# Optimization experiments

Measured on AMD Instinct MI355X. Metric: run time of the kernel, lower is better.

The kernel has to match this reference:

```python
import jax, jax.numpy as jnp
import numpy as np
from jax import lax

B, N, T = 64, 50, 30          # batch, history length, words per title
VOCAB, E = 50000, 300          # vocab size, word emb dim
FN, A, G, K = 400, 200, 400, 3 # filter_num, attention_dim, gru_unit, window size
USERS = 50000


def setup_inputs() -> dict:
    key = jax.random.key(0)
    ks = jax.random.split(key, 12)
    return {
        "user_id": jax.random.randint(ks[0], (B,), 0, USERS),
        "history_title": jax.random.randint(ks[1], (B, N, T), 0, VOCAB),
        "history_length": jax.random.randint(ks[2], (B,), 1, N + 1),
        "word_emb": jax.random.normal(ks[3], (VOCAB, E), jnp.float32) * 0.02,
        "conv_w": jax.random.normal(ks[4], (K, E, FN), jnp.float32) * 0.05,  # WIO layout
        "conv_b": jnp.zeros((FN,), jnp.float32),
        "v": jax.random.normal(ks[5], (FN, A), jnp.float32) * 0.05,
        "vb": jnp.zeros((A,), jnp.float32),
        "q": jax.random.normal(ks[6], (A, 1), jnp.float32) * 0.05,
        "user_emb": jax.random.normal(ks[7], (USERS, G), jnp.float32) * 0.02,
        "W_ih": jax.random.normal(ks[8], (3 * G, FN), jnp.float32) * 0.05,
        "W_hh": jax.random.normal(ks[9], (3 * G, G), jnp.float32) * 0.05,
        "b_ih": jnp.zeros((3 * G,), jnp.float32),
        "b_hh": jnp.zeros((3 * G,), jnp.float32),
    }


def _news_encode(history_title, word_emb, conv_w, conv_b, v, vb, q):
    # word embedding lookup: [B, N, T, E] (dropout is identity in eval mode)
    W = word_emb[history_title]
    # Conv1d over the word axis, padding=1 keeps length T
    x = W.reshape(B * N, T, E)
    C = lax.conv_general_dilated(
        x, conv_w, window_strides=(1,), padding=[(1, 1)],
        dimension_numbers=("NWC", "WIO", "NWC")) + conv_b
    C = jax.nn.relu(C).reshape(B, N, T, FN)
    # additive attention scores
    a = jnp.tanh(jnp.einsum("bntf,fa->bnta", C, v) + vb)
    a = jnp.einsum("bnta,ao->bnt", a, q)  # q: [A,1] -> squeeze
    # original uses Softmax(dim=0) on a [n, t] per sample => over the n-titles axis
    alpha = jax.nn.softmax(a, axis=1)
    # e[i] = alpha[i] @ C[i]: weighted sum over words -> [B, N, FN]
    return jnp.einsum("bnt,bntf->bnf", alpha, C)


def _gru(news_embed, h0, lengths, W_ih, W_hh, b_ih, b_hh):
    # packed_padded semantics: h stops updating once step >= length
    xs = jnp.swapaxes(news_embed, 0, 1)                 # [N, B, FN]
    mask = jnp.arange(N)[:, None] < lengths[None, :]    # [N, B]

    def step(h, inp):
        x_t, m = inp
        gx = x_t @ W_ih.T + b_ih                        # [B, 3G]
        gh = h @ W_hh.T + b_hh
        xr, xz, xn = jnp.split(gx, 3, axis=-1)
        hr, hz, hn = jnp.split(gh, 3, axis=-1)
        r = jax.nn.sigmoid(xr + hr)
        z = jax.nn.sigmoid(xz + hz)
        n = jnp.tanh(xn + r * hn)
        h_new = (1.0 - z) * n + z * h
        h = jnp.where(m[:, None], h_new, h)
        return h, None

    h_final, _ = lax.scan(step, h0, (xs, mask))
    return h_final


def reference(user_id, history_title, history_length, word_emb, conv_w, conv_b,
              v, vb, q, user_emb, W_ih, W_hh, b_ih, b_hh):
    news_embed = _news_encode(history_title, word_emb, conv_w, conv_b, v, vb, q)
    h0 = user_emb[user_id]                              # [B, G]
    return _gru(news_embed, h0, history_length, W_ih, W_hh, b_ih, b_hh)
```

## Files before the change

kernel.cpp:

```cpp
#include <hip/hip_runtime.h>
#include <hip/hip_bf16.h>

#define BB 64
#define NN 50
#define TT 30
#define EE 300
#define FN 400
#define AA 200
#define GG 400

typedef __attribute__((ext_vector_type(8))) short bf16x8;
typedef __attribute__((ext_vector_type(4))) float f32x4;

__global__ void k_pack_whh(const float* __restrict__ Whh, float* __restrict__ Wpack) {
  int idx = blockIdx.x * 256 + threadIdx.x;
  if (idx < 8 * 400 * 150) {
    int jl = idx % 150;
    int g = (idx / 150) % 400;
    int gc = idx / (150 * 400);
    int gate = jl / 50, gl = jl - gate * 50;
    int j = gate * 400 + gc * 50 + gl;
    Wpack[idx] = Whh[j * 400 + g];
  }
}

__global__ void k_prep_emb(const float* __restrict__ w, __hip_bfloat16* __restrict__ o) {
  long i = (long)blockIdx.x * 256 + threadIdx.x;
  if (i < (long)50000 * 320) {
    int row = (int)(i / 320), c = (int)(i % 320);
    o[i] = __float2bfloat16(c < EE ? w[(long)row * EE + c] : 0.f);
  }
}

__global__ void k_prep_wt(const float* __restrict__ cw, __hip_bfloat16* __restrict__ o) {
  int i = blockIdx.x * 256 + threadIdx.x;
  if (i < 448 * 960) {
    int f = i / 960, kk = i % 960;
    int ko = kk / 320, e = kk % 320;
    float val = (f < FN && e < EE) ? cw[(ko * EE + e) * FN + f] : 0.f;
    o[i] = __float2bfloat16(val);
  }
}

__global__ void k_prep_v(const float* __restrict__ v, __hip_bfloat16* __restrict__ o) {
  int i = blockIdx.x * 256 + threadIdx.x;
  if (i < 224 * 416) {
    int a = i / 416, f = i % 416;
    o[i] = __float2bfloat16((a < AA && f < FN) ? v[f * AA + a] : 0.f);
  }
}

__global__ void k_prep_qvb(const float* __restrict__ q, const float* __restrict__ vb,
                           float* __restrict__ qp, float* __restrict__ vbp) {
  int i = threadIdx.x;
  if (i < 224) {
    qp[i]  = i < AA ? q[i]  : 0.f;
    vbp[i] = i < AA ? vb[i] : 0.f;
  }
}

__global__ void k_prep_wih(const float* __restrict__ w, __hip_bfloat16* __restrict__ o) {
  int i = blockIdx.x * 256 + threadIdx.x;
  if (i < 1344 * 416) {
    int j = i / 416, f = i % 416;
    o[i] = __float2bfloat16((j < 1200 && f < 400) ? w[j * 400 + f] : 0.f);
  }
}

__global__ __launch_bounds__(512) void k_conv(
    const int* __restrict__ title, const __hip_bfloat16* __restrict__ emb,
    const __hip_bfloat16* __restrict__ WT, const float* __restrict__ conv_b,
    __hip_bfloat16* __restrict__ C)
{
  __shared__ __align__(16) ushort Alds[128 * 40];
  __shared__ __align__(16) ushort Blds[448 * 40];
  __shared__ int words[120];
  const int g = blockIdx.x;
  const int tid = threadIdx.x;
  const int lane = tid & 63;
  const int wid = tid >> 6;
  const int wm = wid >> 2;
  const int wn = wid & 3;
  const int l15 = lane & 15;
  const int l4 = lane >> 4;

  if (tid < 120) words[tid] = title[g * 120 + tid];

  f32x4 acc[4][7];
  {
    float bias[7];
#pragma unroll
    for (int nt = 0; nt < 7; ++nt) {
      int f = wn * 112 + nt * 16 + l15;
      bias[nt] = (f < FN) ? conv_b[f] : 0.f;
    }
#pragma unroll
    for (int mt = 0; mt < 4; ++mt)
#pragma unroll
      for (int nt = 0; nt < 7; ++nt) {
        acc[mt][nt][0] = bias[nt]; acc[mt][nt][1] = bias[nt];
        acc[mt][nt][2] = bias[nt]; acc[mt][nt][3] = bias[nt];
      }
  }
  __syncthreads();

  const int ar = tid >> 2, ac = tid & 3;
  const int ati = ar >> 5, at = ar & 31;

  for (int ko = 0; ko < 3; ++ko) {
    int w = at + ko - 1;
    const bool valid = (w >= 0 && w < TT);
    const ushort* asrc = valid ? (const ushort*)emb + (size_t)words[ati * 30 + w] * 320
                               : (const ushort*)emb;
    for (int ks = 0; ks < 10; ++ks) {
      uint4 av = make_uint4(0u, 0u, 0u, 0u);
      if (valid) av = *(const uint4*)(asrc + ks * 32 + ac * 8);
      *(uint4*)(&Alds[ar * 40 + ac * 8]) = av;
      for (int idx = tid; idx < 1792; idx += 512) {
        int f = idx >> 2, c = idx & 3;
        *(uint4*)(&Blds[f * 40 + c * 8]) =
            *(const uint4*)((const ushort*)WT + f * 960 + ko * 320 + ks * 32 + c * 8);
      }
      __syncthreads();
      bf16x8 af[4];
#pragma unroll
      for (int mt = 0; mt < 4; ++mt)
        af[mt] = *(const bf16x8*)(&Alds[(wm * 64 + mt * 16 + l15) * 40 + l4 * 8]);
#pragma unroll
      for (int nt = 0; nt < 7; ++nt) {
        bf16x8 bfr = *(const bf16x8*)(&Blds[(wn * 112 + nt * 16 + l15) * 40 + l4 * 8]);
#pragma unroll
        for (int mt = 0; mt < 4; ++mt)
          acc[mt][nt] = __builtin_amdgcn_mfma_f32_16x16x32_bf16(af[mt], bfr, acc[mt][nt], 0, 0, 0);
      }
      __syncthreads();
    }
  }

#pragma unroll
  for (int mt = 0; mt < 4; ++mt) {
    int rowb = wm * 64 + mt * 16 + l4 * 4;
    int ti = rowb >> 5;
    int tb = rowb & 31;
#pragma unroll
    for (int nt = 0; nt < 7; ++nt) {
      int f = wn * 112 + nt * 16 + l15;
      if (f < 416) {
#pragma unroll
        for (int r = 0; r < 4; ++r) {
          int t = tb + r;
          if (t < TT) {
            float vv = fmaxf(acc[mt][nt][r], 0.f);
            C[((size_t)(g * 4 + ti) * 30 + t) * 416 + f] = __float2bfloat16(vv);
          }
        }
      }
    }
  }
}

__global__ __launch_bounds__(512) void k_attn(
    const __hip_bfloat16* __restrict__ C, const __hip_bfloat16* __restrict__ vT,
    const float* __restrict__ vbp, const float* __restrict__ qp,
    float* __restrict__ score)
{
  __shared__ __align__(16) ushort Clds[256 * 40];
  __shared__ __align__(16) ushort Vlds[224 * 40];
  __shared__ float sred[2][256];
  const int tid = threadIdx.x;
  const int lane = tid & 63, wid = tid >> 6;
  const int wm = wid >> 1, wn = wid & 1;
  const int l15 = lane & 15, l4 = lane >> 4;
  const size_t row0 = (size_t)blockIdx.x * 256;

  f32x4 acc[4][7];
  float ql[7];
#pragma unroll
  for (int nt = 0; nt < 7; ++nt) {
    int a = wn * 112 + nt * 16 + l15;
    ql[nt] = qp[a];
    float vbv = vbp[a];
#pragma unroll
    for (int mt = 0; mt < 4; ++mt) {
      acc[mt][nt][0] = vbv; acc[mt][nt][1] = vbv;
      acc[mt][nt][2] = vbv; acc[mt][nt][3] = vbv;
    }
  }

  for (int ks = 0; ks < 13; ++ks) {
    for (int idx = tid; idx < 1024; idx += 512) {
      int r = idx >> 2, c = idx & 3;
      *(uint4*)(&Clds[r * 40 + c * 8]) =
          *(const uint4*)((const ushort*)C + (row0 + r) * 416 + ks * 32 + c * 8);
    }
    for (int idx = tid; idx < 896; idx += 512) {
      int a = idx >> 2, c = idx & 3;
      *(uint4*)(&Vlds[a * 40 + c * 8]) =
          *(const uint4*)((const ushort*)vT + a * 416 + ks * 32 + c * 8);
    }
    __syncthreads();
    bf16x8 cf[4];
#pragma unroll
    for (int mt = 0; mt < 4; ++mt)
      cf[mt] = *(const bf16x8*)(&Clds[(wm * 64 + mt * 16 + l15) * 40 + l4 * 8]);
#pragma unroll
    for (int nt = 0; nt < 7; ++nt) {
      bf16x8 vf = *(const bf16x8*)(&Vlds[(wn * 112 + nt * 16 + l15) * 40 + l4 * 8]);
#pragma unroll
      for (int mt = 0; mt < 4; ++mt)
        acc[mt][nt] = __builtin_amdgcn_mfma_f32_16x16x32_bf16(cf[mt], vf, acc[mt][nt], 0, 0, 0);
    }
    __syncthreads();
  }

  float sums[4][4];
#pragma unroll
  for (int mt = 0; mt < 4; ++mt)
#pragma unroll
    for (int r = 0; r < 4; ++r) sums[mt][r] = 0.f;
#pragma unroll
  for (int mt = 0; mt < 4; ++mt)
#pragma unroll
    for (int nt = 0; nt < 7; ++nt)
#pragma unroll
      for (int r = 0; r < 4; ++r)
        sums[mt][r] += tanhf(acc[mt][nt][r]) * ql[nt];
#pragma unroll
  for (int mask = 1; mask < 16; mask <<= 1)
#pragma unroll
    for (int mt = 0; mt < 4; ++mt)
#pragma unroll
      for (int r = 0; r < 4; ++r)
        sums[mt][r] += __shfl_xor(sums[mt][r], mask);

  float outv = 0.f;
#pragma unroll
  for (int mt = 0; mt < 4; ++mt)
#pragma unroll
    for (int r = 0; r < 4; ++r)
      if (l15 == mt * 4 + r) outv = sums[mt][r];
  sred[wn][wm * 64 + (l15 >> 2) * 16 + l4 * 4 + (l15 & 3)] = outv;
  __syncthreads();
  if (tid < 256) score[row0 + tid] = sred[0][tid] + sred[1][tid];
}

__global__ void k2_softmax_n(const float* __restrict__ score, float* __restrict__ alpha) {
  int i = blockIdx.x * 256 + threadIdx.x;
  if (i >= BB * TT) return;
  int b = i / TT, t = i - b * TT;
  int base = b * (NN * TT) + t;
  float m = -1e30f;
  for (int n = 0; n < NN; ++n) m = fmaxf(m, score[base + n * TT]);
  float s = 0.f;
  for (int n = 0; n < NN; ++n) s += __expf(score[base + n * TT] - m);
  float inv = 1.f / s;
  for (int n = 0; n < NN; ++n)
    alpha[base + n * TT] = __expf(score[base + n * TT] - m) * inv;
}

__global__ __launch_bounds__(256) void k3_wsum(
    const float* __restrict__ alpha, const __hip_bfloat16* __restrict__ C,
    __hip_bfloat16* __restrict__ Ebf) {
  __shared__ float al[TT];
  const int bn = blockIdx.x;
  const int tid = threadIdx.x;
  if (tid < TT) al[tid] = alpha[bn * TT + tid];
  __syncthreads();
  for (int f = tid; f < 416; f += 256) {
    float s = 0.f;
    if (f < FN) {
#pragma unroll
      for (int t = 0; t < TT; ++t)
        s = fmaf(al[t], __bfloat162float(C[((size_t)bn * TT + t) * 416 + f]), s);
    }
    Ebf[(size_t)bn * 416 + f] = __float2bfloat16(s);
  }
}

__global__ __launch_bounds__(512) void k4_gx_mfma(
    const __hip_bfloat16* __restrict__ Ebf,
    const __hip_bfloat16* __restrict__ Wih,
    const float* __restrict__ b_ih,
    float* __restrict__ gx)
{
  __shared__ __align__(16) ushort Alds[128 * 40];
  __shared__ __align__(16) ushort Blds[448 * 40];
  const int tid = threadIdx.x;
  const int lane = tid & 63, wid = tid >> 6;
  const int wm = wid >> 2, wn = wid & 3;
  const int l15 = lane & 15, l4 = lane >> 4;
  const int mb = blockIdx.x / 3;
  const int nb = blockIdx.x - mb * 3;
  const int row0 = mb * 128;
  const int n0 = nb * 448;

  f32x4 acc[4][7];
#pragma unroll
  for (int nt = 0; nt < 7; ++nt) {
    int j = n0 + wn * 112 + nt * 16 + l15;
    float bj = (j < 1200) ? b_ih[j] : 0.f;
#pragma unroll
    for (int mt = 0; mt < 4; ++mt) {
      acc[mt][nt][0] = bj; acc[mt][nt][1] = bj;
      acc[mt][nt][2] = bj; acc[mt][nt][3] = bj;
    }
  }

  const int ar = tid >> 2, ac = tid & 3;
  for (int ks = 0; ks < 13; ++ks) {
    *(uint4*)(&Alds[ar * 40 + ac * 8]) =
        *(const uint4*)((const ushort*)Ebf + (size_t)(row0 + ar) * 416 + ks * 32 + ac * 8);
    for (int idx = tid; idx < 1792; idx += 512) {
      int r = idx >> 2, c = idx & 3;
      *(uint4*)(&Blds[r * 40 + c * 8]) =
          *(const uint4*)((const ushort*)Wih + (size_t)(n0 + r) * 416 + ks * 32 + c * 8);
    }
    __syncthreads();
    bf16x8 af[4];
#pragma unroll
    for (int mt = 0; mt < 4; ++mt)
      af[mt] = *(const bf16x8*)(&Alds[(wm * 64 + mt * 16 + l15) * 40 + l4 * 8]);
#pragma unroll
    for (int nt = 0; nt < 7; ++nt) {
      bf16x8 bfr = *(const bf16x8*)(&Blds[(wn * 112 + nt * 16 + l15) * 40 + l4 * 8]);
#pragma unroll
      for (int mt = 0; mt < 4; ++mt)
        acc[mt][nt] = __builtin_amdgcn_mfma_f32_16x16x32_bf16(af[mt], bfr, acc[mt][nt], 0, 0, 0);
    }
    __syncthreads();
  }

#pragma unroll
  for (int mt = 0; mt < 4; ++mt) {
    int row = row0 + wm * 64 + mt * 16 + l4 * 4;
#pragma unroll
    for (int nt = 0; nt < 7; ++nt) {
      int j = n0 + wn * 112 + nt * 16 + l15;
      if (j < 1200) {
#pragma unroll
        for (int r = 0; r < 4; ++r)
          gx[(size_t)(row + r) * 1200 + j] = acc[mt][nt][r];
      }
    }
  }
}

__global__ void k5_init(const int* __restrict__ user_id,
                        const float* __restrict__ user_emb,
                        float* __restrict__ h0) {
  int idx = blockIdx.x * 256 + threadIdx.x;
  if (idx < BB * GG) {
    int b = idx / GG, g = idx - b * GG;
    h0[idx] = user_emb[(long)user_id[b] * GG + g];
  }
}

__global__ __launch_bounds__(256) void k5_step(
    const float* __restrict__ h_prev, float* __restrict__ h_next,
    const float* __restrict__ Wpack, const float* __restrict__ b_hh,
    const float* __restrict__ gx, const int* __restrict__ hist_len, int step)
{
  const int gc = blockIdx.x & 7;
  const int bg = blockIdx.x >> 3;
  const int tid = threadIdx.x;
  __shared__ float hl[2][GG];
  __shared__ float ghl[2][3][50];

  for (int i = tid; i < 2 * GG; i += 256) {
    int b = i / GG, g = i - b * GG;
    hl[b][g] = h_prev[(2 * bg + b) * GG + g];
  }
  __syncthreads();

  if (tid < 150) {
    float acc0 = 0.f, acc1 = 0.f;
    const float* wp = Wpack + (size_t)gc * 400 * 150 + tid;
#pragma unroll 8
    for (int g = 0; g < GG; ++g) {
      float w = wp[g * 150];
      acc0 = fmaf(hl[0][g], w, acc0);
      acc1 = fmaf(hl[1][g], w, acc1);
    }
    int gate = tid / 50, gl = tid - gate * 50;
    float bb = b_hh[gate * 400 + gc * 50 + gl];
    ghl[0][gate][gl] = acc0 + bb;
    ghl[1][gate][gl] = acc1 + bb;
  }
  __syncthreads();

  if (tid < 100) {
    int b = tid / 50, gl = tid - (tid / 50) * 50;
    int babs = 2 * bg + b;
    int g = gc * 50 + gl;
    const float* gxp = gx + ((size_t)babs * NN + step) * 1200;
    float xr = gxp[g], xz = gxp[400 + g], xn = gxp[800 + g];
    float hr = ghl[b][0][gl], hz = ghl[b][1][gl], hn = ghl[b][2][gl];
    float r = 1.f / (1.f + __expf(-(xr + hr)));
    float z = 1.f / (1.f + __expf(-(xz + hz)));
    float nv = tanhf(xn + r * hn);
    float hold = hl[b][g];
    float hnew = (1.f - z) * nv + z * hold;
    h_next[babs * GG + g] = (step < hist_len[babs]) ? hnew : hold;
  }
}

__global__ void k5_out(const float* __restrict__ h, float* __restrict__ out) {
  int idx = blockIdx.x * 256 + threadIdx.x;
  if (idx < BB * GG) out[idx] = h[idx];
}

extern "C" void kernel_launch(void* const* d_in, const int* in_sizes, int n_in,
                              void* d_out, int out_size, void* d_ws, size_t ws_size,
                              hipStream_t stream) {
  const int*   user_id   = (const int*)d_in[0];
  const int*   title     = (const int*)d_in[1];
  const int*   hist_len  = (const int*)d_in[2];
  const float* word_emb  = (const float*)d_in[3];
  const float* conv_w    = (const float*)d_in[4];
  const float* conv_b    = (const float*)d_in[5];
  const float* v         = (const float*)d_in[6];
  const float* vb        = (const float*)d_in[7];
  const float* q         = (const float*)d_in[8];
  const float* user_emb  = (const float*)d_in[9];
  const float* W_ih      = (const float*)d_in[10];
  const float* W_hh      = (const float*)d_in[11];
  const float* b_ih      = (const float*)d_in[12];
  const float* b_hh      = (const float*)d_in[13];
  float* out = (float*)d_out;

  char* ws = (char*)d_ws;
  size_t off = 0;
  auto take = [&](size_t bytes) {
    char* p = ws + off;
    off = (off + bytes + 255) & ~(size_t)255;
    return p;
  };
  __hip_bfloat16* C      = (__hip_bfloat16*)take((size_t)BB * NN * TT * 416 * 2);
  float* score  = (float*)take((size_t)BB * NN * TT * 4);
  float* alpha  = (float*)take((size_t)BB * NN * TT * 4);
  __hip_bfloat16* Ebf    = (__hip_bfloat16*)take((size_t)BB * NN * 416 * 2);
  __hip_bfloat16* Wih_bf = (__hip_bfloat16*)take((size_t)1344 * 416 * 2);
  float* Wpack  = (float*)take((size_t)8 * 400 * 150 * 4);
  float* gx     = (float*)take((size_t)BB * NN * 1200 * 4);
  float* h0     = (float*)take((size_t)BB * GG * 4);
  float* h1     = (float*)take((size_t)BB * GG * 4);
  __hip_bfloat16* emb_bf = (__hip_bfloat16*)take((size_t)50000 * 320 * 2);
  __hip_bfloat16* WT     = (__hip_bfloat16*)take((size_t)448 * 960 * 2);
  __hip_bfloat16* vT     = (__hip_bfloat16*)take((size_t)224 * 416 * 2);
  float* qp     = (float*)take(224 * 4);
  float* vbp    = (float*)take(224 * 4);
  (void)ws_size;

  k_pack_whh<<<(8 * 400 * 150 + 255) / 256, 256, 0, stream>>>(W_hh, Wpack);
  k_prep_emb<<<(50000 * 320 + 255) / 256, 256, 0, stream>>>(word_emb, emb_bf);
  k_prep_wt<<<(448 * 960 + 255) / 256, 256, 0, stream>>>(conv_w, WT);
  k_prep_v<<<(224 * 416 + 255) / 256, 256, 0, stream>>>(v, vT);
  k_prep_qvb<<<1, 256, 0, stream>>>(q, vb, qp, vbp);
  k_prep_wih<<<(1344 * 416 + 255) / 256, 256, 0, stream>>>(W_ih, Wih_bf);

  k_conv<<<BB * NN / 4, 512, 0, stream>>>(title, emb_bf, WT, conv_b, C);
  k_attn<<<BB * NN * TT / 256, 512, 0, stream>>>(C, vT, vbp, qp, score);
  k2_softmax_n<<<(BB * TT + 255) / 256, 256, 0, stream>>>(score, alpha);
  k3_wsum<<<BB * NN, 256, 0, stream>>>(alpha, C, Ebf);
  k4_gx_mfma<<<75, 512, 0, stream>>>(Ebf, Wih_bf, b_ih, gx);

  k5_init<<<(BB * GG + 255) / 256, 256, 0, stream>>>(user_id, user_emb, h0);
  float* hbuf[2] = {h0, h1};
  for (int step = 0; step < NN; ++step) {
    k5_step<<<256, 256, 0, stream>>>(hbuf[step & 1], hbuf[(step + 1) & 1],
                                     Wpack, b_hh, gx, hist_len, step);
  }
  k5_out<<<(BB * GG + 255) / 256, 256, 0, stream>>>(h0, out);
}
```

Measured before the change: 961.7 us.

## Stage title embeddings once in LDS and stream conv weights directly from global

The conv kernel now loads the 32-row padded embedding block for two titles into LDS once and reuses it across all three kernel offsets by shifting the row slot. This replaces re-gathering embeddings for each offset and k-step. Conv weights are repacked into an MFMA-fragment-friendly layout and read straight into registers from global/L2, which removes the B tile staging and the per-step barriers. Blocks shrink to 256 threads covering 2 titles each, doubling the grid. The trade-off is heavier global weight traffic per block and more register pressure from the prefetched B fragments.

```diff
diff --git a/kernel.cpp b/kernel.cpp
--- a/kernel.cpp
+++ b/kernel.cpp
@@ -32,11 +32,11 @@
   }
 }
 
-__global__ void k_prep_wt(const float* __restrict__ cw, __hip_bfloat16* __restrict__ o) {
+__global__ void k_prep_wt2(const float* __restrict__ cw, __hip_bfloat16* __restrict__ o) {
   int i = blockIdx.x * 256 + threadIdx.x;
-  if (i < 448 * 960) {
-    int f = i / 960, kk = i % 960;
-    int ko = kk / 320, e = kk % 320;
+  if (i < 30 * 448 * 32) {
+    int kk = i & 31, f = (i >> 5) % 448, s = i / (448 * 32);
+    int ko = s / 10, e = (s - ko * 10) * 32 + kk;
     float val = (f < FN && e < EE) ? cw[(ko * EE + e) * FN + f] : 0.f;
     o[i] = __float2bfloat16(val);
   }
@@ -67,91 +67,87 @@
   }
 }
 
-__global__ __launch_bounds__(512) void k_conv(
+__global__ __launch_bounds__(256) void k_conv(
     const int* __restrict__ title, const __hip_bfloat16* __restrict__ emb,
-    const __hip_bfloat16* __restrict__ WT, const float* __restrict__ conv_b,
+    const __hip_bfloat16* __restrict__ WT2, const float* __restrict__ conv_b,
     __hip_bfloat16* __restrict__ C)
 {
-  __shared__ __align__(16) ushort Alds[128 * 40];
-  __shared__ __align__(16) ushort Blds[448 * 40];
-  __shared__ int words[120];
+  __shared__ __align__(16) ushort E[2][34][328];
+  __shared__ int words[60];
   const int g = blockIdx.x;
   const int tid = threadIdx.x;
-  const int lane = tid & 63;
-  const int wid = tid >> 6;
-  const int wm = wid >> 2;
-  const int wn = wid & 3;
-  const int l15 = lane & 15;
-  const int l4 = lane >> 4;
-
-  if (tid < 120) words[tid] = title[g * 120 + tid];
+  const int lane = tid & 63, wn = tid >> 6;
+  const int l15 = lane & 15, l4 = lane >> 4;
+
+  if (tid < 60) words[tid] = title[g * 60 + tid];
+  __syncthreads();
+
+  for (int idx = tid; idx < 2400; idx += 256) {
+    int row = idx / 40, c = idx - row * 40;
+    int ti = row / 30, w = row - ti * 30;
+    const ushort* src = (const ushort*)emb + (size_t)words[row] * 320 + c * 8;
+    *(uint4*)(&E[ti][w + 1][c * 8]) = *(const uint4*)src;
+  }
+  for (int idx = tid; idx < 320; idx += 256) {
+    int z = idx / 40, c = idx - z * 40;
+    int ti = z >> 2, sl = z & 3;
+    int slot = (sl == 0) ? 0 : 30 + sl;
+    *(uint4*)(&E[ti][slot][c * 8]) = make_uint4(0u, 0u, 0u, 0u);
+  }
+  __syncthreads();
 
   f32x4 acc[4][7];
-  {
-    float bias[7];
-#pragma unroll
-    for (int nt = 0; nt < 7; ++nt) {
-      int f = wn * 112 + nt * 16 + l15;
-      bias[nt] = (f < FN) ? conv_b[f] : 0.f;
-    }
-#pragma unroll
-    for (int mt = 0; mt < 4; ++mt)
-#pragma unroll
-      for (int nt = 0; nt < 7; ++nt) {
-        acc[mt][nt][0] = bias[nt]; acc[mt][nt][1] = bias[nt];
-        acc[mt][nt][2] = bias[nt]; acc[mt][nt][3] = bias[nt];
+#pragma unroll
+  for (int nt = 0; nt < 7; ++nt) {
+    int f = wn * 112 + nt * 16 + l15;
+    float bj = (f < FN) ? conv_b[f] : 0.f;
+#pragma unroll
+    for (int mt = 0; mt < 4; ++mt) {
+      acc[mt][nt][0] = bj; acc[mt][nt][1] = bj;
+      acc[mt][nt][2] = bj; acc[mt][nt][3] = bj;
+    }
+  }
+
+  const ushort* Bbase = (const ushort*)WT2 + (size_t)(wn * 112 + l15) * 32 + l4 * 8;
+
+#pragma unroll
+  for (int ko = 0; ko < 3; ++ko) {
+#pragma unroll
+    for (int ks = 0; ks < 10; ++ks) {
+      const int s = ko * 10 + ks;
+      bf16x8 bq[7];
+#pragma unroll
+      for (int nt = 0; nt < 7; ++nt)
+        bq[nt] = *(const bf16x8*)(Bbase + (size_t)s * 14336 + nt * 512);
+      bf16x8 af[4];
+#pragma unroll
+      for (int mt = 0; mt < 4; ++mt) {
+        int row = mt * 16 + l15;
+        int ti = row >> 5, slot = (row & 31) + ko;
+        af[mt] = *(const bf16x8*)(&E[ti][slot][ks * 32 + l4 * 8]);
       }
-  }
-  __syncthreads();
-
-  const int ar = tid >> 2, ac = tid & 3;
-  const int ati = ar >> 5, at = ar & 31;
-
-  for (int ko = 0; ko < 3; ++ko) {
-    int w = at + ko - 1;
-    const bool valid = (w >= 0 && w < TT);
-    const ushort* asrc = valid ? (const ushort*)emb + (size_t)words[ati * 30 + w] * 320
-                               : (const ushort*)emb;
-    for (int ks = 0; ks < 10; ++ks) {
-      uint4 av = make_uint4(0u, 0u, 0u, 0u);
-      if (valid) av = *(const uint4*)(asrc + ks * 32 + ac * 8);
-      *(uint4*)(&Alds[ar * 40 + ac * 8]) = av;
-      for (int idx = tid; idx < 1792; idx += 512) {
-        int f = idx >> 2, c = idx & 3;
-        *(uint4*)(&Blds[f * 40 + c * 8]) =
-            *(const uint4*)((const ushort*)WT + f * 960 + ko * 320 + ks * 32 + c * 8);
-      }
-      __syncthreads();
-      bf16x8 af[4];
-#pragma unroll
-      for (int mt = 0; mt < 4; ++mt)
-        af[mt] = *(const bf16x8*)(&Alds[(wm * 64 + mt * 16 + l15) * 40 + l4 * 8]);
-#pragma unroll
-      for (int nt = 0; nt < 7; ++nt) {
-        bf16x8 bfr = *(const bf16x8*)(&Blds[(wn * 112 + nt * 16 + l15) * 40 + l4 * 8]);
+#pragma unroll
+      for (int nt = 0; nt < 7; ++nt)
 #pragma unroll
         for (int mt = 0; mt < 4; ++mt)
-          acc[mt][nt] = __builtin_amdgcn_mfma_f32_16x16x32_bf16(af[mt], bfr, acc[mt][nt], 0, 0, 0);
-      }
-      __syncthreads();
+          acc[mt][nt] = __builtin_amdgcn_mfma_f32_16x16x32_bf16(af[mt], bq[nt], acc[mt][nt], 0, 0, 0);
     }
   }
 
 #pragma unroll
   for (int mt = 0; mt < 4; ++mt) {
-    int rowb = wm * 64 + mt * 16 + l4 * 4;
-    int ti = rowb >> 5;
-    int tb = rowb & 31;
+    int rowb = mt * 16 + l4 * 4;
 #pragma unroll
     for (int nt = 0; nt < 7; ++nt) {
       int f = wn * 112 + nt * 16 + l15;
       if (f < 416) {
 #pragma unroll
         for (int r = 0; r < 4; ++r) {
-          int t = tb + r;
+          int row = rowb + r;
+          int ti = row >> 5, t = row & 31;
           if (t < TT) {
             float vv = fmaxf(acc[mt][nt][r], 0.f);
-            C[((size_t)(g * 4 + ti) * 30 + t) * 416 + f] = __float2bfloat16(vv);
+            C[((size_t)(g * 2 + ti) * 30 + t) * 416 + f] = __float2bfloat16(vv);
           }
         }
       }
@@ -445,7 +441,7 @@
   float* h0     = (float*)take((size_t)BB * GG * 4);
   float* h1     = (float*)take((size_t)BB * GG * 4);
   __hip_bfloat16* emb_bf = (__hip_bfloat16*)take((size_t)50000 * 320 * 2);
-  __hip_bfloat16* WT     = (__hip_bfloat16*)take((size_t)448 * 960 * 2);
+  __hip_bfloat16* WT2    = (__hip_bfloat16*)take((size_t)30 * 448 * 32 * 2);
   __hip_bfloat16* vT     = (__hip_bfloat16*)take((size_t)224 * 416 * 2);
   float* qp     = (float*)take(224 * 4);
   float* vbp    = (float*)take(224 * 4);
@@ -453,12 +449,12 @@
 
   k_pack_whh<<<(8 * 400 * 150 + 255) / 256, 256, 0, stream>>>(W_hh, Wpack);
   k_prep_emb<<<(50000 * 320 + 255) / 256, 256, 0, stream>>>(word_emb, emb_bf);
-  k_prep_wt<<<(448 * 960 + 255) / 256, 256, 0, stream>>>(conv_w, WT);
+  k_prep_wt2<<<(30 * 448 * 32 + 255) / 256, 256, 0, stream>>>(conv_w, WT2);
   k_prep_v<<<(224 * 416 + 255) / 256, 256, 0, stream>>>(v, vT);
   k_prep_qvb<<<1, 256, 0, stream>>>(q, vb, qp, vbp);
   k_prep_wih<<<(1344 * 416 + 255) / 256, 256, 0, stream>>>(W_ih, Wih_bf);
 
-  k_conv<<<BB * NN / 4, 512, 0, stream>>>(title, emb_bf, WT, conv_b, C);
+  k_conv<<<BB * NN / 2, 256, 0, stream>>>(title, emb_bf, WT2, conv_b, C);
   k_attn<<<BB * NN * TT / 256, 512, 0, stream>>>(C, vT, vbp, qp, score);
   k2_softmax_n<<<(BB * TT + 255) / 256, 256, 0, stream>>>(score, alpha);
   k3_wsum<<<BB * NN, 256, 0, stream>>>(alpha, C, Ebf);
```

Measured after the change: 889.9 us. 7.5% less time.
